# Kernel optimization log

Measured on AMD Instinct MI355X. Metric: run time of the kernel, lower is better.

## Reference

```python
import jax, jax.numpy as jnp
import numpy as np

N_NODES = 100000
N_EDGES = 3200000
BATCH = 256
NUM_TAU = 4
ORDER = 8


def setup_inputs() -> dict:
    key = jax.random.key(0)
    k1, k2, k3, k4, k5 = jax.random.split(key, 5)
    coeffs = jax.random.normal(k1, (NUM_TAU, ORDER + 1), dtype=jnp.float32)
    # positive weights mimicking a degree-normalized adjacency
    edge_weights = jax.random.uniform(k2, (N_EDGES,), dtype=jnp.float32)
    src = jax.random.randint(k3, (N_EDGES,), 0, N_NODES, dtype=jnp.int32)
    dst = jax.random.randint(k4, (N_EDGES,), 0, N_NODES, dtype=jnp.int32)
    batch_indices = jax.random.randint(k5, (BATCH,), 0, N_NODES, dtype=jnp.int64)
    return {
        "coeffs": coeffs,
        "edge_weights": edge_weights,
        "src": src,
        "dst": dst,
        "batch_indices": batch_indices,
        "n_nodes": N_NODES,
    }


def reference(coeffs, edge_weights, src, dst, batch_indices, n_nodes):
    # coeffs: [num_tau, order+1]; edge list defines sparse normalized adjacency.
    B = batch_indices.shape[0]
    order = coeffs.shape[1] - 1
    # _create_batch: one-hot columns, monome[batch_indices[j], j] = 1
    monome = jnp.zeros((n_nodes, B), dtype=coeffs.dtype)
    monome = monome.at[batch_indices, jnp.arange(B)].set(1.0)
    # out[t] = sum_k coeffs[t, k] * A^k @ one_hot
    out = coeffs[:, 0][:, None, None] * monome[None, :, :]
    for k in range(order):
        # SpMM: monome_new[d] += w_e * monome[s] for each edge e=(s,d)
        monome = jax.ops.segment_sum(
            edge_weights[:, None] * monome[src], dst, num_segments=n_nodes
        )
        out = out + coeffs[:, k + 1][:, None, None] * monome[None, :, :]
    return out
```

## Files before the change

kernel.cpp:

```cpp
#include <hip/hip_runtime.h>

#define N_NODES 100000
#define BATCH   256
#define NUM_TAU 4
#define ORDER   8
#define NB      ((size_t)N_NODES * BATCH)

__device__ __forceinline__ unsigned short f2bf(float f) {
    unsigned int u = __float_as_uint(f);
    u += 0x7FFFu + ((u >> 16) & 1u);
    return (unsigned short)(u >> 16);
}
__device__ __forceinline__ float bf2f(unsigned short h) {
    return __uint_as_float((unsigned int)h << 16);
}


__global__ void hist_kernel(const int* __restrict__ dst, int* __restrict__ counts, int E) {
    int e = blockIdx.x * blockDim.x + threadIdx.x;
    if (e < E) atomicAdd(&counts[dst[e]], 1);
}

__global__ void alloc_kernel(const int* __restrict__ counts, int* __restrict__ rowStart,
                             int* __restrict__ cursor, int* __restrict__ totalCursor) {
    int n = blockIdx.x * blockDim.x + threadIdx.x;
    if (n < N_NODES) {
        int len = counts[n];
        int start = atomicAdd(totalCursor, len);
        rowStart[n] = start;
        cursor[n] = start;
    }
}

__global__ void scatter_kernel(const int* __restrict__ src, const int* __restrict__ dst,
                               const float* __restrict__ w, int* __restrict__ cursor,
                               int2* __restrict__ csr_pair, int E) {
    int e = blockIdx.x * blockDim.x + threadIdx.x;
    if (e < E) {
        int d = dst[e];
        int p = atomicAdd(&cursor[d], 1);
        int2 pr;
        pr.x = src[e];
        pr.y = __float_as_int(w[e]);
        csr_pair[p] = pr;
    }
}


__global__ void colmap_kernel(const int* __restrict__ bi, int* __restrict__ col_of_node,
                              int* __restrict__ next_dup) {
    int j = threadIdx.x;
    int prev = atomicExch(&col_of_node[bi[j]], j);
    next_dup[j] = prev;
}

__global__ void m1_edges_kernel(const int* __restrict__ src, const int* __restrict__ dst,
                                const float* __restrict__ w,
                                const int* __restrict__ col_of_node,
                                const int* __restrict__ next_dup,
                                float* __restrict__ m1, int* __restrict__ flag, int E) {
    int e = blockIdx.x * blockDim.x + threadIdx.x;
    if (e >= E) return;
    int j = col_of_node[src[e]];
    if (j < 0) return;
    float we = w[e];
    int d = dst[e];
    flag[d] = 1;
    size_t rb = (size_t)d * BATCH;
    while (j >= 0) {
        atomicAdd(&m1[rb + j], we);
        j = next_dup[j];
    }
}

__global__ void spmm_k2(const float* __restrict__ m1, unsigned short* __restrict__ m2,
                        const int* __restrict__ rowStart, const int* __restrict__ counts,
                        const int2* __restrict__ csr_pair, const int* __restrict__ flag) {
    int wave = threadIdx.x >> 6;
    int lane = threadIdx.x & 63;
    int node = blockIdx.x * 4 + wave;
    if (node >= N_NODES) return;
    int col0 = lane * 4;

    int start = rowStart[node];
    int len   = counts[node];

    float4 acc = make_float4(0.f, 0.f, 0.f, 0.f);
    for (int i = 0; i < len; ++i) {
        int2 pr = csr_pair[start + i];
        if (flag[pr.x]) {
            float w = __int_as_float(pr.y);
            float4 v = *(const float4*)(m1 + (size_t)pr.x * BATCH + col0);
            acc.x += w * v.x; acc.y += w * v.y; acc.z += w * v.z; acc.w += w * v.w;
        }
    }
    ushort4 o;
    o.x = f2bf(acc.x); o.y = f2bf(acc.y); o.z = f2bf(acc.z); o.w = f2bf(acc.w);
    *(ushort4*)(m2 + (size_t)node * BATCH + col0) = o;
}

__global__ void spmm_bf(const unsigned short* __restrict__ min_, unsigned short* __restrict__ mout,
                        const int* __restrict__ rowStart, const int* __restrict__ counts,
                        const int2* __restrict__ csr_pair) {
    int wave = threadIdx.x >> 6;
    int lane = threadIdx.x & 63;
    int node = blockIdx.x * 4 + wave;
    if (node >= N_NODES) return;
    int col0 = lane * 4;

    int start = rowStart[node];
    int len   = counts[node];

    float4 acc = make_float4(0.f, 0.f, 0.f, 0.f);
    int i = 0;
    for (; i + 8 <= len; i += 8) {
        int2 pr[8];
        #pragma unroll
        for (int u = 0; u < 8; ++u) pr[u] = csr_pair[start + i + u];
        ushort4 v[8];
        #pragma unroll
        for (int u = 0; u < 8; ++u)
            v[u] = *(const ushort4*)(min_ + (size_t)pr[u].x * BATCH + col0);
        #pragma unroll
        for (int u = 0; u < 8; ++u) {
            float w = __int_as_float(pr[u].y);
            acc.x += w * bf2f(v[u].x);
            acc.y += w * bf2f(v[u].y);
            acc.z += w * bf2f(v[u].z);
            acc.w += w * bf2f(v[u].w);
        }
    }
    for (; i < len; ++i) {
        int2 pr = csr_pair[start + i];
        float w = __int_as_float(pr.y);
        ushort4 v = *(const ushort4*)(min_ + (size_t)pr.x * BATCH + col0);
        acc.x += w * bf2f(v.x);
        acc.y += w * bf2f(v.y);
        acc.z += w * bf2f(v.z);
        acc.w += w * bf2f(v.w);
    }
    ushort4 o;
    o.x = f2bf(acc.x); o.y = f2bf(acc.y); o.z = f2bf(acc.z); o.w = f2bf(acc.w);
    *(ushort4*)(mout + (size_t)node * BATCH + col0) = o;
}

__global__ void combine_bf(float* __restrict__ out, const unsigned short* __restrict__ m28,
                           const float* __restrict__ coeffs, const int* __restrict__ bi) {
    size_t tid = (size_t)blockIdx.x * blockDim.x + threadIdx.x;
    size_t base = tid * 4;
    if (base >= NB) return;
    int node = (int)(base >> 8);
    int j0   = (int)(base & 255);

    float4 p[ORDER];
    p[0] = *(const float4*)(out + base);
    #pragma unroll
    for (int k = 2; k <= ORDER; ++k) {
        ushort4 v = *(const ushort4*)(m28 + (size_t)(k - 2) * NB + base);
        p[k - 1] = make_float4(bf2f(v.x), bf2f(v.y), bf2f(v.z), bf2f(v.w));
    }

    float oh[4];
    #pragma unroll
    for (int i = 0; i < 4; ++i) oh[i] = (bi[j0 + i] == node) ? 1.0f : 0.0f;

    #pragma unroll
    for (int t = 0; t < NUM_TAU; ++t) {
        float c0 = coeffs[t * (ORDER + 1)];
        float4 o = make_float4(c0 * oh[0], c0 * oh[1], c0 * oh[2], c0 * oh[3]);
        #pragma unroll
        for (int k = 1; k <= ORDER; ++k) {
            float c = coeffs[t * (ORDER + 1) + k];
            o.x += c * p[k - 1].x;
            o.y += c * p[k - 1].y;
            o.z += c * p[k - 1].z;
            o.w += c * p[k - 1].w;
        }
        *(float4*)(out + (size_t)t * NB + base) = o;
    }
}


__global__ void spmm_half(const float* __restrict__ min_, float* __restrict__ mout,
                          const int* __restrict__ rowStart, const int* __restrict__ counts,
                          const int2* __restrict__ csr_pair, int colOff) {
    int wave = threadIdx.x >> 6;
    int lane = threadIdx.x & 63;
    int node = blockIdx.x * 4 + wave;
    if (node >= N_NODES) return;
    int c = colOff + lane * 2;
    int start = rowStart[node];
    int len   = counts[node];
    float2 acc = make_float2(0.f, 0.f);
    int i = 0;
    for (; i + 8 <= len; i += 8) {
        int2 pr[8];
        #pragma unroll
        for (int u = 0; u < 8; ++u) pr[u] = csr_pair[start + i + u];
        float2 v[8];
        #pragma unroll
        for (int u = 0; u < 8; ++u)
            v[u] = *(const float2*)(min_ + (size_t)pr[u].x * BATCH + c);
        #pragma unroll
        for (int u = 0; u < 8; ++u) {
            float w = __int_as_float(pr[u].y);
            acc.x += w * v[u].x;
            acc.y += w * v[u].y;
        }
    }
    for (; i < len; ++i) {
        int2 pr = csr_pair[start + i];
        float w = __int_as_float(pr.y);
        float2 v = *(const float2*)(min_ + (size_t)pr.x * BATCH + c);
        acc.x += w * v.x;
        acc.y += w * v.y;
    }
    *(float2*)(mout + (size_t)node * BATCH + c) = acc;
}

__global__ void combine_kernel(float* __restrict__ out, const float* __restrict__ m14,
                               const float* __restrict__ coeffs, const int* __restrict__ bi) {
    size_t tid = (size_t)blockIdx.x * blockDim.x + threadIdx.x;
    size_t base = tid * 4;
    if (base >= NB) return;
    int node = (int)(base >> 8);
    int j0   = (int)(base & 255);
    float4 p[ORDER];
    #pragma unroll
    for (int k = 1; k <= 4; ++k)
        p[k - 1] = *(const float4*)(m14 + (size_t)(k - 1) * NB + base);
    #pragma unroll
    for (int k = 5; k <= 8; ++k)
        p[k - 1] = *(const float4*)(out + (size_t)(k - 5) * NB + base);
    float oh[4];
    #pragma unroll
    for (int i = 0; i < 4; ++i) oh[i] = (bi[j0 + i] == node) ? 1.0f : 0.0f;
    #pragma unroll
    for (int t = 0; t < NUM_TAU; ++t) {
        float c0 = coeffs[t * (ORDER + 1)];
        float4 o = make_float4(c0 * oh[0], c0 * oh[1], c0 * oh[2], c0 * oh[3]);
        #pragma unroll
        for (int k = 1; k <= ORDER; ++k) {
            float c = coeffs[t * (ORDER + 1) + k];
            o.x += c * p[k - 1].x;
            o.y += c * p[k - 1].y;
            o.z += c * p[k - 1].z;
            o.w += c * p[k - 1].w;
        }
        *(float4*)(out + (size_t)t * NB + base) = o;
    }
}

extern "C" void kernel_launch(void* const* d_in, const int* in_sizes, int n_in,
                              void* d_out, int out_size, void* d_ws, size_t ws_size,
                              hipStream_t stream) {
    const float* coeffs = (const float*)d_in[0];
    const float* ew     = (const float*)d_in[1];
    const int*   src    = (const int*)d_in[2];
    const int*   dst    = (const int*)d_in[3];
    const int*   bi     = (const int*)d_in[4];
    const int E = in_sizes[1];

    float* out = (float*)d_out;

    auto align_up = [](uintptr_t v, uintptr_t a) { return (v + a - 1) & ~(a - 1); };

    uintptr_t p0 = (uintptr_t)d_ws;
    int* counts      = (int*)p0;  p0 += (size_t)N_NODES * 4;  p0 = align_up(p0, 256);
    int* rowStart    = (int*)p0;  p0 += (size_t)N_NODES * 4;  p0 = align_up(p0, 256);
    int* cursor      = (int*)p0;  p0 += (size_t)N_NODES * 4;  p0 = align_up(p0, 256);
    int* totalCursor = (int*)p0;  p0 += 256;
    int* col_of_node = (int*)p0;  p0 += (size_t)N_NODES * 4;  p0 = align_up(p0, 256);
    int* next_dup    = (int*)p0;  p0 += 1024;                 p0 = align_up(p0, 256);
    int* flag        = (int*)p0;  p0 += (size_t)N_NODES * 4;  p0 = align_up(p0, 256);
    int2* csr_pair   = (int2*)p0; p0 += (size_t)E * 8;        p0 = align_up(p0, 256);
    void* big        = (void*)p0;
    size_t big_bytes = ((uintptr_t)d_ws + ws_size > p0) ? ((uintptr_t)d_ws + ws_size - p0) : 0;

    int eb = (E + 255) / 256;
    int nodeGrid = (N_NODES + 3) / 4;
    int cgrid = (int)((NB / 4 + 255) / 256);

    hipMemsetAsync(counts, 0, (size_t)N_NODES * 4, stream);
    hipMemsetAsync(totalCursor, 0, 4, stream);

    hist_kernel<<<eb, 256, 0, stream>>>(dst, counts, E);
    alloc_kernel<<<(N_NODES + 255) / 256, 256, 0, stream>>>(counts, rowStart, cursor, totalCursor);
    scatter_kernel<<<eb, 256, 0, stream>>>(src, dst, ew, cursor, csr_pair, E);

    if (big_bytes >= 7 * NB * 2) {
        unsigned short* m28 = (unsigned short*)big;
        float* m1 = out;

        hipMemsetAsync(col_of_node, 0xFF, (size_t)N_NODES * 4, stream);
        hipMemsetAsync(flag, 0, (size_t)N_NODES * 4, stream);
        hipMemsetAsync(m1, 0, NB * 4, stream);

        colmap_kernel<<<1, 256, 0, stream>>>(bi, col_of_node, next_dup);
        m1_edges_kernel<<<eb, 256, 0, stream>>>(src, dst, ew, col_of_node, next_dup,
                                                m1, flag, E);
        spmm_k2<<<nodeGrid, 256, 0, stream>>>(m1, m28, rowStart, counts, csr_pair, flag);
        for (int k = 3; k <= ORDER; ++k) {
            spmm_bf<<<nodeGrid, 256, 0, stream>>>(m28 + (size_t)(k - 3) * NB,
                                                  m28 + (size_t)(k - 2) * NB,
                                                  rowStart, counts, csr_pair);
        }
        combine_bf<<<cgrid, 256, 0, stream>>>(out, m28, coeffs, bi);
    } else {
        float* fbig = (float*)big;
        float* mpow[ORDER + 1];
        for (int k = 1; k <= 4; ++k) mpow[k] = fbig + (size_t)(k - 1) * NB;
        for (int k = 5; k <= 8; ++k) mpow[k] = out + (size_t)(k - 5) * NB;

        hipMemsetAsync(col_of_node, 0xFF, (size_t)N_NODES * 4, stream);
        hipMemsetAsync(flag, 0, (size_t)N_NODES * 4, stream);
        hipMemsetAsync(mpow[1], 0, NB * 4, stream);
        colmap_kernel<<<1, 256, 0, stream>>>(bi, col_of_node, next_dup);
        m1_edges_kernel<<<eb, 256, 0, stream>>>(src, dst, ew, col_of_node, next_dup,
                                                mpow[1], flag, E);
        for (int h = 0; h < 2; ++h) {
            int colOff = h * 128;
            for (int k = 2; k <= ORDER; ++k) {
                spmm_half<<<nodeGrid, 256, 0, stream>>>(mpow[k - 1], mpow[k],
                                                        rowStart, counts, csr_pair, colOff);
            }
        }
        combine_kernel<<<cgrid, 256, 0, stream>>>(out, fbig, coeffs, bi);
    }
}
```

Before: 2.076 ms.

## Build CSR with ordered prefix scan and two-pass bucketed scatter

Replaces the atomic-based row allocation with a three-stage prefix scan, so row starts follow node order. The edge scatter becomes two passes: edges are first grouped by 1024-node destination bucket, then placed into their final rows. The goal is more local, better-coalesced writes for the CSR build and SpMM rows laid out in node order. In exchange it adds several small kernel launches and an extra pass over the edges through a temporary buffer stored in the workspace.

```diff
diff --git a/kernel.cpp b/kernel.cpp
--- a/kernel.cpp
+++ b/kernel.cpp
@@ -5,6 +5,8 @@
 #define NUM_TAU 4
 #define ORDER   8
 #define NB      ((size_t)N_NODES * BATCH)
+#define NBUK    98
+#define NBLK    391
 
 __device__ __forceinline__ unsigned short f2bf(float f) {
     unsigned int u = __float_as_uint(f);
@@ -21,28 +23,95 @@
     if (e < E) atomicAdd(&counts[dst[e]], 1);
 }
 
-__global__ void alloc_kernel(const int* __restrict__ counts, int* __restrict__ rowStart,
-                             int* __restrict__ cursor, int* __restrict__ totalCursor) {
-    int n = blockIdx.x * blockDim.x + threadIdx.x;
-    if (n < N_NODES) {
-        int len = counts[n];
-        int start = atomicAdd(totalCursor, len);
-        rowStart[n] = start;
-        cursor[n] = start;
-    }
-}
-
-__global__ void scatter_kernel(const int* __restrict__ src, const int* __restrict__ dst,
-                               const float* __restrict__ w, int* __restrict__ cursor,
-                               int2* __restrict__ csr_pair, int E) {
+__global__ void scan1(const int* __restrict__ counts, int* __restrict__ blockSum) {
+    __shared__ int s[256];
+    int n = blockIdx.x * 256 + threadIdx.x;
+    s[threadIdx.x] = (n < N_NODES) ? counts[n] : 0;
+    __syncthreads();
+    for (int st = 128; st > 0; st >>= 1) {
+        if (threadIdx.x < st) s[threadIdx.x] += s[threadIdx.x + st];
+        __syncthreads();
+    }
+    if (threadIdx.x == 0) blockSum[blockIdx.x] = s[0];
+}
+
+__global__ void scan2(int* __restrict__ blockSum) {
+    __shared__ int s[512];
+    int t = threadIdx.x;
+    int v = (t < NBLK) ? blockSum[t] : 0;
+    s[t] = v;
+    __syncthreads();
+    for (int st = 1; st < 512; st <<= 1) {
+        int u = (t >= st) ? s[t - st] : 0;
+        __syncthreads();
+        s[t] += u;
+        __syncthreads();
+    }
+    if (t < NBLK) blockSum[t] = s[t] - v;
+}
+
+__global__ void scan3(const int* __restrict__ counts, const int* __restrict__ blockSumEx,
+                      int* __restrict__ rowStart) {
+    __shared__ int s[256];
+    int n = blockIdx.x * 256 + threadIdx.x;
+    int v = (n < N_NODES) ? counts[n] : 0;
+    s[threadIdx.x] = v;
+    __syncthreads();
+    for (int st = 1; st < 256; st <<= 1) {
+        int u = (threadIdx.x >= st) ? s[threadIdx.x - st] : 0;
+        __syncthreads();
+        s[threadIdx.x] += u;
+        __syncthreads();
+    }
+    if (n < N_NODES) rowStart[n] = blockSumEx[blockIdx.x] + s[threadIdx.x] - v;
+}
+
+__global__ void initcur_kernel(const int* __restrict__ rowStart, int* __restrict__ cursor,
+                               int* __restrict__ bcur) {
+    int n = blockIdx.x * 256 + threadIdx.x;
+    if (n < N_NODES) cursor[n] = rowStart[n];
+    if (n < NBUK) bcur[n] = rowStart[n << 10];
+}
+
+#define EPT 16
+__global__ void bucketize_kernel(const int* __restrict__ src, const int* __restrict__ dst,
+                                 const float* __restrict__ w, int* __restrict__ bcur,
+                                 int2* __restrict__ isw, int* __restrict__ idn, int E) {
+    __shared__ int cnt[NBUK], base[NBUK], off[NBUK];
+    int e0 = blockIdx.x * (256 * EPT);
+    for (int i = threadIdx.x; i < NBUK; i += 256) { cnt[i] = 0; off[i] = 0; }
+    __syncthreads();
+    #pragma unroll
+    for (int i = 0; i < EPT; ++i) {
+        int e = e0 + i * 256 + threadIdx.x;
+        if (e < E) atomicAdd(&cnt[dst[e] >> 10], 1);
+    }
+    __syncthreads();
+    for (int i = threadIdx.x; i < NBUK; i += 256) {
+        int c = cnt[i];
+        base[i] = c ? atomicAdd(&bcur[i], c) : 0;
+    }
+    __syncthreads();
+    #pragma unroll
+    for (int i = 0; i < EPT; ++i) {
+        int e = e0 + i * 256 + threadIdx.x;
+        if (e < E) {
+            int d = dst[e];
+            int b = d >> 10;
+            int p = base[b] + atomicAdd(&off[b], 1);
+            isw[p] = make_int2(src[e], __float_as_int(w[e]));
+            idn[p] = d;
+        }
+    }
+}
+
+__global__ void place_kernel(const int2* __restrict__ isw, const int* __restrict__ idn,
+                             int* __restrict__ cursor, int2* __restrict__ csr_pair, int E) {
     int e = blockIdx.x * blockDim.x + threadIdx.x;
     if (e < E) {
-        int d = dst[e];
+        int d = idn[e];
         int p = atomicAdd(&cursor[d], 1);
-        int2 pr;
-        pr.x = src[e];
-        pr.y = __float_as_int(w[e]);
-        csr_pair[p] = pr;
+        csr_pair[p] = isw[e];
     }
 }
 
@@ -269,7 +338,8 @@
     int* counts      = (int*)p0;  p0 += (size_t)N_NODES * 4;  p0 = align_up(p0, 256);
     int* rowStart    = (int*)p0;  p0 += (size_t)N_NODES * 4;  p0 = align_up(p0, 256);
     int* cursor      = (int*)p0;  p0 += (size_t)N_NODES * 4;  p0 = align_up(p0, 256);
-    int* totalCursor = (int*)p0;  p0 += 256;
+    int* blockSum    = (int*)p0;  p0 += (size_t)NBLK * 4;     p0 = align_up(p0, 256);
+    int* bcur        = (int*)p0;  p0 += (size_t)NBUK * 4;     p0 = align_up(p0, 256);
     int* col_of_node = (int*)p0;  p0 += (size_t)N_NODES * 4;  p0 = align_up(p0, 256);
     int* next_dup    = (int*)p0;  p0 += 1024;                 p0 = align_up(p0, 256);
     int* flag        = (int*)p0;  p0 += (size_t)N_NODES * 4;  p0 = align_up(p0, 256);
@@ -281,14 +351,25 @@
     int nodeGrid = (N_NODES + 3) / 4;
     int cgrid = (int)((NB / 4 + 255) / 256);
 
+    bool schemeA = (big_bytes >= 7 * NB * 2);
+    uintptr_t ibase;
+    if (schemeA) ibase = (uintptr_t)big + 5 * NB * 2;
+    else         ibase = (uintptr_t)big + 3 * NB * 4;
+    ibase = align_up(ibase, 256);
+    int2* isw = (int2*)ibase;
+    int*  idn = (int*)(ibase + (size_t)E * 8);
+
     hipMemsetAsync(counts, 0, (size_t)N_NODES * 4, stream);
-    hipMemsetAsync(totalCursor, 0, 4, stream);
-
     hist_kernel<<<eb, 256, 0, stream>>>(dst, counts, E);
-    alloc_kernel<<<(N_NODES + 255) / 256, 256, 0, stream>>>(counts, rowStart, cursor, totalCursor);
-    scatter_kernel<<<eb, 256, 0, stream>>>(src, dst, ew, cursor, csr_pair, E);
-
-    if (big_bytes >= 7 * NB * 2) {
+    scan1<<<NBLK, 256, 0, stream>>>(counts, blockSum);
+    scan2<<<1, 512, 0, stream>>>(blockSum);
+    scan3<<<NBLK, 256, 0, stream>>>(counts, blockSum, rowStart);
+    initcur_kernel<<<NBLK, 256, 0, stream>>>(rowStart, cursor, bcur);
+    bucketize_kernel<<<(E + 256 * EPT - 1) / (256 * EPT), 256, 0, stream>>>(
+        src, dst, ew, bcur, isw, idn, E);
+    place_kernel<<<eb, 256, 0, stream>>>(isw, idn, cursor, csr_pair, E);
+
+    if (schemeA) {
         unsigned short* m28 = (unsigned short*)big;
         float* m1 = out;
 
```

After: 2.022 ms. -2.6%, faster.
